# Performance work log

Measured on AMD Instinct MI355X. Metric: run time of the kernel, lower is better.

## Reference

```python
import jax, jax.numpy as jnp
import numpy as np

DF = 16
B, D, H, W = 2, 64, 64, 64


def _shift(a, axis, s):
    """Return a shifted so out[i] = a[i+s] along `axis`, zero-padded."""
    pad = [(0, 0)] * a.ndim
    pad[axis] = (1, 1)
    ap = jnp.pad(a, pad)
    idx = [slice(None)] * a.ndim
    idx[axis] = slice(1 + s, 1 + s + a.shape[axis])
    return ap[tuple(idx)]


def _image_grad(x, sum_axis):
    """Faithful replica of ImageGradient's (buggy) dense kernel.

    Uses only input channel 1; central difference along W; summed over the
    3 taps along `sum_axis` (1=D for pos==1, 2=H for pos==2); result is
    identical across all output channels.
    x: [B, C, D, H, W] -> [B, C, D, H, W]
    """
    s = x[:, 1]  # [B, D, H, W]
    g = 0.5 * (_shift(s, 3, 1) - _shift(s, 3, -1))  # d/dW central diff
    g3 = _shift(g, sum_axis, -1) + g + _shift(g, sum_axis, 1)
    return jnp.broadcast_to(g3[:, None], x.shape)


def _pconv(x, w, b):
    """nn.Conv3d(cin, cout, 1, padding=1): zero-pad spatial dims then 1x1x1 conv."""
    xp = jnp.pad(x, ((0, 0), (0, 0), (1, 1), (1, 1), (1, 1)))
    return jnp.einsum('bcdhw,oc->bodhw', xp, w) + b[None, :, None, None, None]


def setup_inputs() -> dict:
    key = jax.random.key(0)
    ks = jax.random.split(key, 8)
    p = jax.random.normal(ks[0], (B, DF, D, H, W), dtype=jnp.float32)
    q = jax.random.normal(ks[1], (B, DF, D, H, W), dtype=jnp.float32)
    W1 = jax.random.normal(ks[2], (DF, 6 * DF), dtype=jnp.float32) / np.sqrt(6 * DF)
    b1 = jax.random.normal(ks[3], (DF,), dtype=jnp.float32) * 0.01
    W2 = jax.random.normal(ks[4], (DF, DF), dtype=jnp.float32) / np.sqrt(DF)
    b2 = jax.random.normal(ks[5], (DF,), dtype=jnp.float32) * 0.01
    W3 = jax.random.normal(ks[6], (1, DF), dtype=jnp.float32) / np.sqrt(DF)
    b3 = jax.random.normal(ks[7], (1,), dtype=jnp.float32) * 0.01
    return {"p": p, "q": q, "W1": W1, "b1": b1, "W2": W2, "b2": b2, "W3": W3, "b3": b3}


def reference(p, q, W1, b1, W2, b2, W3, b3):
    dpx = _image_grad(p, 1)  # gradx: pos==1, sum over kd (D axis)
    dpy = _image_grad(p, 2)  # grady: pos==2, sum over kh (H axis)
    dqx = _image_grad(q, 1)
    dqy = _image_grad(q, 2)
    h = jnp.concatenate([p, dpx, dpy, q, dqx, dqy], axis=1)  # [B, 6*DF, D, H, W]
    h = jax.nn.relu(_pconv(h, W1, b1))  # [B, DF, D+2, H+2, W+2]
    h = jax.nn.relu(_pconv(h, W2, b2))  # [B, DF, D+4, H+4, W+4]
    h = jax.nn.relu(_pconv(h, W3, b3))  # [B, 1, D+6, H+6, W+6]
    return (h, p, dpx, dpy, q, dqx, dqy)
```

## Files before the change

### kernel.cpp

```cpp
#include <hip/hip_runtime.h>

#define N3   (64*64*64)
#define NO   70
#define NO2  (NO*NO)
#define NO3  (NO*NO*NO)
#define OH   (2*NO3)
#define SZ   (2*16*N3)

typedef __attribute__((ext_vector_type(4))) float f4;

__device__ __forceinline__ float relu(float x){ return x > 0.f ? x : 0.f; }

__global__ __launch_bounds__(256) void ham_interior(
    const float* __restrict__ p, const float* __restrict__ q,
    const float* __restrict__ W1, const float* __restrict__ b1,
    const float* __restrict__ W2, const float* __restrict__ b2,
    const float* __restrict__ W3, const float* __restrict__ b3p,
    float* __restrict__ out)
{
    __shared__ float WpT[16][16];
    __shared__ float WqT[16][16];
    __shared__ float W2l[16][16];
    __shared__ float b1l[16], b2l[16], W3l[16];
    __shared__ float s1x[16], s1y[16], s2x[16], s2y[16];

    int t = threadIdx.x;
    {
        int o = t >> 4, c = t & 15;
        WpT[c][o] = W1[o*96 + c];
        WqT[c][o] = W1[o*96 + 48 + c];
        W2l[o][c] = W2[o*16 + c];
    }
    if (t < 16) {
        b1l[t] = b1[t]; b2l[t] = b2[t]; W3l[t] = W3[t];
        float ax=0.f, ay=0.f, bx=0.f, by=0.f;
        #pragma unroll
        for (int j = 0; j < 16; ++j) {
            ax += W1[t*96 + 16 + j];
            ay += W1[t*96 + 32 + j];
            bx += W1[t*96 + 64 + j];
            by += W1[t*96 + 80 + j];
        }
        s1x[t]=ax; s1y[t]=ay; s2x[t]=bx; s2y[t]=by;
    }
    __syncthreads();

    int i  = blockIdx.x * 256 + t;
    int w4 = i & 15;  int w0 = w4 << 2;
    int r  = i >> 4;
    int h0 = r & 63;  r >>= 6;
    int d0 = r & 63;  int b = r >> 6;

    float b3v = b3p[0];

    const float* ps = p + (b*16 + 1)*N3;
    const float* qs = q + (b*16 + 1)*N3;

    auto row6 = [&](const float* s, int dd, int hh, float rr[6]) {
        if ((unsigned)dd >= 64u || (unsigned)hh >= 64u) {
            #pragma unroll
            for (int j = 0; j < 6; ++j) rr[j] = 0.f;
            return;
        }
        const float* rp = s + dd*4096 + hh*64 + w0;
        f4 v = *(const f4*)rp;
        rr[1]=v[0]; rr[2]=v[1]; rr[3]=v[2]; rr[4]=v[3];
        rr[0] = (w4 > 0)  ? rp[-1] : 0.f;
        rr[5] = (w4 < 15) ? rp[4]  : 0.f;
    };

    float dpx[4], dpy[4], dqx[4], dqy[4];
    {
        float rc[6], ra[6], rb[6], gc[4];
        row6(ps, d0,   h0,   rc);
        row6(ps, d0-1, h0,   ra);
        row6(ps, d0+1, h0,   rb);
        #pragma unroll
        for (int j = 0; j < 4; ++j) gc[j]  = 0.5f*(rc[j+2]-rc[j]);
        #pragma unroll
        for (int j = 0; j < 4; ++j) dpx[j] = 0.5f*(ra[j+2]-ra[j]) + gc[j] + 0.5f*(rb[j+2]-rb[j]);
        row6(ps, d0, h0-1, ra);
        row6(ps, d0, h0+1, rb);
        #pragma unroll
        for (int j = 0; j < 4; ++j) dpy[j] = 0.5f*(ra[j+2]-ra[j]) + gc[j] + 0.5f*(rb[j+2]-rb[j]);

        row6(qs, d0,   h0,   rc);
        row6(qs, d0-1, h0,   ra);
        row6(qs, d0+1, h0,   rb);
        #pragma unroll
        for (int j = 0; j < 4; ++j) gc[j]  = 0.5f*(rc[j+2]-rc[j]);
        #pragma unroll
        for (int j = 0; j < 4; ++j) dqx[j] = 0.5f*(ra[j+2]-ra[j]) + gc[j] + 0.5f*(rb[j+2]-rb[j]);
        row6(qs, d0, h0-1, ra);
        row6(qs, d0, h0+1, rb);
        #pragma unroll
        for (int j = 0; j < 4; ++j) dqy[j] = 0.5f*(ra[j+2]-ra[j]) + gc[j] + 0.5f*(rb[j+2]-rb[j]);
    }

    float y1[4][16];
    #pragma unroll
    for (int j = 0; j < 4; ++j)
        #pragma unroll
        for (int o = 0; o < 16; ++o)
            y1[j][o] = b1l[o] + s1x[o]*dpx[j] + s1y[o]*dpy[j]
                              + s2x[o]*dqx[j] + s2y[o]*dqy[j];

    int ibase = b*16*N3 + d0*4096 + h0*64 + w0;

    float* outp  = out + OH;
    float* outdx = out + OH + SZ;
    float* outdy = out + OH + 2*SZ;
    float* outq  = out + OH + 3*SZ;
    float* outqx = out + OH + 4*SZ;
    float* outqy = out + OH + 5*SZ;

    #pragma unroll
    for (int c = 0; c < 16; ++c) {
        f4 pc = *(const f4*)(p + ibase + c*N3);
        f4 qc = *(const f4*)(q + ibase + c*N3);
        __builtin_nontemporal_store(pc, (f4*)(outp + ibase + c*N3));
        __builtin_nontemporal_store(qc, (f4*)(outq + ibase + c*N3));
        #pragma unroll
        for (int o = 0; o < 16; ++o) {
            float wp = WpT[c][o], wq = WqT[c][o];
            #pragma unroll
            for (int j = 0; j < 4; ++j)
                y1[j][o] += wp*pc[j] + wq*qc[j];
        }
    }

    f4 vdx, vdy, vqx, vqy;
    #pragma unroll
    for (int j = 0; j < 4; ++j) { vdx[j]=dpx[j]; vdy[j]=dpy[j]; vqx[j]=dqx[j]; vqy[j]=dqy[j]; }
    #pragma unroll
    for (int c = 0; c < 16; ++c) {
        __builtin_nontemporal_store(vdx, (f4*)(outdx + ibase + c*N3));
        __builtin_nontemporal_store(vdy, (f4*)(outdy + ibase + c*N3));
        __builtin_nontemporal_store(vqx, (f4*)(outqx + ibase + c*N3));
        __builtin_nontemporal_store(vqy, (f4*)(outqy + ibase + c*N3));
    }

    int obase = b*NO3 + (d0+3)*NO2 + (h0+3)*NO + (w0+3);
    #pragma unroll
    for (int j = 0; j < 4; ++j) {
        float acc = b3v;
        #pragma unroll
        for (int o = 0; o < 16; ++o) {
            float a2 = b2l[o];
            #pragma unroll
            for (int c = 0; c < 16; ++c) a2 += W2l[o][c]*relu(y1[j][c]);
            acc += W3l[o]*relu(a2);
        }
        out[obase + j] = relu(acc);
    }
}

__global__ __launch_bounds__(256) void ham_border(
    const float* __restrict__ b1, const float* __restrict__ W2,
    const float* __restrict__ b2, const float* __restrict__ W3,
    const float* __restrict__ b3p, float* __restrict__ out)
{
    int i = blockIdx.x * 256 + threadIdx.x;
    if (i >= OH) return;

    int b = i / NO3;
    int r = i - b*NO3;
    int d = r / NO2; r -= d*NO2;
    int h = r / NO;
    int w = r - h*NO;
    (void)b;

    if ((unsigned)(d-3) < 64u && (unsigned)(h-3) < 64u && (unsigned)(w-3) < 64u) return;

    float b3v = b3p[0];
    float val;
    if ((unsigned)(d-1) >= 68u || (unsigned)(h-1) >= 68u || (unsigned)(w-1) >= 68u) {
        val = relu(b3v);
    } else if ((unsigned)(d-2) >= 66u || (unsigned)(h-2) >= 66u || (unsigned)(w-2) >= 66u) {
        float acc = b3v;
        #pragma unroll
        for (int o = 0; o < 16; ++o) acc += W3[o]*relu(b2[o]);
        val = relu(acc);
    } else {
        float acc = b3v;
        #pragma unroll
        for (int o = 0; o < 16; ++o) {
            float a2 = b2[o];
            #pragma unroll
            for (int c = 0; c < 16; ++c) a2 += W2[o*16 + c]*relu(b1[c]);
            acc += W3[o]*relu(a2);
        }
        val = relu(acc);
    }
    out[i] = val;
}

extern "C" void kernel_launch(void* const* d_in, const int* in_sizes, int n_in,
                              void* d_out, int out_size, void* d_ws, size_t ws_size,
                              hipStream_t stream) {
    const float* p  = (const float*)d_in[0];
    const float* q  = (const float*)d_in[1];
    const float* W1 = (const float*)d_in[2];
    const float* b1 = (const float*)d_in[3];
    const float* W2 = (const float*)d_in[4];
    const float* b2 = (const float*)d_in[5];
    const float* W3 = (const float*)d_in[6];
    const float* b3 = (const float*)d_in[7];
    float* out = (float*)d_out;

    ham_interior<<<512, 256, 0, stream>>>(p, q, W1, b1, W2, b2, W3, b3, out);
    ham_border<<<(OH + 255)/256, 256, 0, stream>>>(b1, W2, b2, W3, b3, out);
}
```

Baseline: 380.5 us.

## Fuse interior and border kernels into one launch and restructure store order

Merges the border-fill kernel into the interior kernel by giving the extra blocks a separate code path, so only one launch is issued. It also switches the nontemporal stores to plain stores, reorders work so the gradient outputs are written before the p/q copy loop to shorten register live ranges, and adds an occupancy hint of 4 blocks per CU to launch bounds. The aim is to remove the second launch's overhead and tail, and to get more waves in flight on the store-bound interior. Plain stores may pollute the cache, and the occupancy hint may cause register spills given the 64-float accumulator.

```diff
diff --git a/kernel.cpp b/kernel.cpp
--- a/kernel.cpp
+++ b/kernel.cpp
@@ -7,24 +7,61 @@
 #define OH   (2*NO3)
 #define SZ   (2*16*N3)
 
+#define INT_BLOCKS 512
+#define BRD_BLOCKS ((OH + 255) / 256)
+
 typedef __attribute__((ext_vector_type(4))) float f4;
 
 __device__ __forceinline__ float relu(float x){ return x > 0.f ? x : 0.f; }
 
-__global__ __launch_bounds__(256) void ham_interior(
+__global__ __launch_bounds__(256, 4) void ham_fused(
     const float* __restrict__ p, const float* __restrict__ q,
     const float* __restrict__ W1, const float* __restrict__ b1,
     const float* __restrict__ W2, const float* __restrict__ b2,
     const float* __restrict__ W3, const float* __restrict__ b3p,
     float* __restrict__ out)
 {
+    int t = threadIdx.x;
+
+    if (blockIdx.x >= INT_BLOCKS) {
+        int i = (blockIdx.x - INT_BLOCKS) * 256 + t;
+        if (i >= OH) return;
+        int r = i % NO3;
+        int d = r / NO2; r -= d*NO2;
+        int h = r / NO;
+        int w = r - h*NO;
+        if ((unsigned)(d-3) < 64u && (unsigned)(h-3) < 64u && (unsigned)(w-3) < 64u)
+            return;
+        float b3v = b3p[0];
+        float val;
+        if ((unsigned)(d-1) >= 68u || (unsigned)(h-1) >= 68u || (unsigned)(w-1) >= 68u) {
+            val = relu(b3v);
+        } else if ((unsigned)(d-2) >= 66u || (unsigned)(h-2) >= 66u || (unsigned)(w-2) >= 66u) {
+            float acc = b3v;
+            #pragma unroll
+            for (int o = 0; o < 16; ++o) acc += W3[o]*relu(b2[o]);
+            val = relu(acc);
+        } else {
+            float acc = b3v;
+            #pragma unroll
+            for (int o = 0; o < 16; ++o) {
+                float a2 = b2[o];
+                #pragma unroll
+                for (int c = 0; c < 16; ++c) a2 += W2[o*16 + c]*relu(b1[c]);
+                acc += W3[o]*relu(a2);
+            }
+            val = relu(acc);
+        }
+        out[i] = val;
+        return;
+    }
+
     __shared__ float WpT[16][16];
     __shared__ float WqT[16][16];
     __shared__ float W2l[16][16];
     __shared__ float b1l[16], b2l[16], W3l[16];
     __shared__ float s1x[16], s1y[16], s2x[16], s2y[16];
 
-    int t = threadIdx.x;
     {
         int o = t >> 4, c = t & 15;
         WpT[c][o] = W1[o*96 + c];
@@ -50,8 +87,6 @@
     int r  = i >> 4;
     int h0 = r & 63;  r >>= 6;
     int d0 = r & 63;  int b = r >> 6;
-
-    float b3v = b3p[0];
 
     const float* ps = p + (b*16 + 1)*N3;
     const float* qs = q + (b*16 + 1)*N3;
@@ -69,77 +104,78 @@
         rr[5] = (w4 < 15) ? rp[4]  : 0.f;
     };
 
-    float dpx[4], dpy[4], dqx[4], dqy[4];
+    float y1[4][16];
+    int ibase = b*16*N3 + d0*4096 + h0*64 + w0;
+
     {
-        float rc[6], ra[6], rb[6], gc[4];
-        row6(ps, d0,   h0,   rc);
-        row6(ps, d0-1, h0,   ra);
-        row6(ps, d0+1, h0,   rb);
-        #pragma unroll
-        for (int j = 0; j < 4; ++j) gc[j]  = 0.5f*(rc[j+2]-rc[j]);
-        #pragma unroll
-        for (int j = 0; j < 4; ++j) dpx[j] = 0.5f*(ra[j+2]-ra[j]) + gc[j] + 0.5f*(rb[j+2]-rb[j]);
-        row6(ps, d0, h0-1, ra);
-        row6(ps, d0, h0+1, rb);
-        #pragma unroll
-        for (int j = 0; j < 4; ++j) dpy[j] = 0.5f*(ra[j+2]-ra[j]) + gc[j] + 0.5f*(rb[j+2]-rb[j]);
-
-        row6(qs, d0,   h0,   rc);
-        row6(qs, d0-1, h0,   ra);
-        row6(qs, d0+1, h0,   rb);
-        #pragma unroll
-        for (int j = 0; j < 4; ++j) gc[j]  = 0.5f*(rc[j+2]-rc[j]);
-        #pragma unroll
-        for (int j = 0; j < 4; ++j) dqx[j] = 0.5f*(ra[j+2]-ra[j]) + gc[j] + 0.5f*(rb[j+2]-rb[j]);
-        row6(qs, d0, h0-1, ra);
-        row6(qs, d0, h0+1, rb);
-        #pragma unroll
-        for (int j = 0; j < 4; ++j) dqy[j] = 0.5f*(ra[j+2]-ra[j]) + gc[j] + 0.5f*(rb[j+2]-rb[j]);
-    }
-
-    float y1[4][16];
-    #pragma unroll
-    for (int j = 0; j < 4; ++j)
-        #pragma unroll
-        for (int o = 0; o < 16; ++o)
-            y1[j][o] = b1l[o] + s1x[o]*dpx[j] + s1y[o]*dpy[j]
-                              + s2x[o]*dqx[j] + s2y[o]*dqy[j];
-
-    int ibase = b*16*N3 + d0*4096 + h0*64 + w0;
-
-    float* outp  = out + OH;
-    float* outdx = out + OH + SZ;
-    float* outdy = out + OH + 2*SZ;
-    float* outq  = out + OH + 3*SZ;
-    float* outqx = out + OH + 4*SZ;
-    float* outqy = out + OH + 5*SZ;
-
-    #pragma unroll
-    for (int c = 0; c < 16; ++c) {
-        f4 pc = *(const f4*)(p + ibase + c*N3);
-        f4 qc = *(const f4*)(q + ibase + c*N3);
-        __builtin_nontemporal_store(pc, (f4*)(outp + ibase + c*N3));
-        __builtin_nontemporal_store(qc, (f4*)(outq + ibase + c*N3));
-        #pragma unroll
-        for (int o = 0; o < 16; ++o) {
-            float wp = WpT[c][o], wq = WqT[c][o];
-            #pragma unroll
-            for (int j = 0; j < 4; ++j)
-                y1[j][o] += wp*pc[j] + wq*qc[j];
-        }
-    }
-
-    f4 vdx, vdy, vqx, vqy;
-    #pragma unroll
-    for (int j = 0; j < 4; ++j) { vdx[j]=dpx[j]; vdy[j]=dpy[j]; vqx[j]=dqx[j]; vqy[j]=dqy[j]; }
-    #pragma unroll
-    for (int c = 0; c < 16; ++c) {
-        __builtin_nontemporal_store(vdx, (f4*)(outdx + ibase + c*N3));
-        __builtin_nontemporal_store(vdy, (f4*)(outdy + ibase + c*N3));
-        __builtin_nontemporal_store(vqx, (f4*)(outqx + ibase + c*N3));
-        __builtin_nontemporal_store(vqy, (f4*)(outqy + ibase + c*N3));
-    }
-
+        f4 vdx, vdy, vqx, vqy;
+        {
+            float rc[6], ra[6], rb[6], gc[4];
+            row6(ps, d0,   h0,   rc);
+            row6(ps, d0-1, h0,   ra);
+            row6(ps, d0+1, h0,   rb);
+            #pragma unroll
+            for (int j = 0; j < 4; ++j) gc[j]  = 0.5f*(rc[j+2]-rc[j]);
+            #pragma unroll
+            for (int j = 0; j < 4; ++j) vdx[j] = 0.5f*(ra[j+2]-ra[j]) + gc[j] + 0.5f*(rb[j+2]-rb[j]);
+            row6(ps, d0, h0-1, ra);
+            row6(ps, d0, h0+1, rb);
+            #pragma unroll
+            for (int j = 0; j < 4; ++j) vdy[j] = 0.5f*(ra[j+2]-ra[j]) + gc[j] + 0.5f*(rb[j+2]-rb[j]);
+
+            row6(qs, d0,   h0,   rc);
+            row6(qs, d0-1, h0,   ra);
+            row6(qs, d0+1, h0,   rb);
+            #pragma unroll
+            for (int j = 0; j < 4; ++j) gc[j]  = 0.5f*(rc[j+2]-rc[j]);
+            #pragma unroll
+            for (int j = 0; j < 4; ++j) vqx[j] = 0.5f*(ra[j+2]-ra[j]) + gc[j] + 0.5f*(rb[j+2]-rb[j]);
+            row6(qs, d0, h0-1, ra);
+            row6(qs, d0, h0+1, rb);
+            #pragma unroll
+            for (int j = 0; j < 4; ++j) vqy[j] = 0.5f*(ra[j+2]-ra[j]) + gc[j] + 0.5f*(rb[j+2]-rb[j]);
+        }
+
+        #pragma unroll
+        for (int j = 0; j < 4; ++j)
+            #pragma unroll
+            for (int o = 0; o < 16; ++o)
+                y1[j][o] = b1l[o] + s1x[o]*vdx[j] + s1y[o]*vdy[j]
+                                  + s2x[o]*vqx[j] + s2y[o]*vqy[j];
+
+        float* outdx = out + OH + SZ;
+        float* outdy = out + OH + 2*SZ;
+        float* outqx = out + OH + 4*SZ;
+        float* outqy = out + OH + 5*SZ;
+        #pragma unroll
+        for (int c = 0; c < 16; ++c) {
+            *(f4*)(outdx + ibase + c*N3) = vdx;
+            *(f4*)(outdy + ibase + c*N3) = vdy;
+            *(f4*)(outqx + ibase + c*N3) = vqx;
+            *(f4*)(outqy + ibase + c*N3) = vqy;
+        }
+    }
+
+    {
+        float* outp = out + OH;
+        float* outq = out + OH + 3*SZ;
+        #pragma unroll
+        for (int c = 0; c < 16; ++c) {
+            f4 pc = *(const f4*)(p + ibase + c*N3);
+            f4 qc = *(const f4*)(q + ibase + c*N3);
+            *(f4*)(outp + ibase + c*N3) = pc;
+            *(f4*)(outq + ibase + c*N3) = qc;
+            #pragma unroll
+            for (int o = 0; o < 16; ++o) {
+                float wp = WpT[c][o], wq = WqT[c][o];
+                #pragma unroll
+                for (int j = 0; j < 4; ++j)
+                    y1[j][o] += wp*pc[j] + wq*qc[j];
+            }
+        }
+    }
+
+    float b3v = b3p[0];
     int obase = b*NO3 + (d0+3)*NO2 + (h0+3)*NO + (w0+3);
     #pragma unroll
     for (int j = 0; j < 4; ++j) {
@@ -153,46 +189,6 @@
         }
         out[obase + j] = relu(acc);
     }
-}
-
-__global__ __launch_bounds__(256) void ham_border(
-    const float* __restrict__ b1, const float* __restrict__ W2,
-    const float* __restrict__ b2, const float* __restrict__ W3,
-    const float* __restrict__ b3p, float* __restrict__ out)
-{
-    int i = blockIdx.x * 256 + threadIdx.x;
-    if (i >= OH) return;
-
-    int b = i / NO3;
-    int r = i - b*NO3;
-    int d = r / NO2; r -= d*NO2;
-    int h = r / NO;
-    int w = r - h*NO;
-    (void)b;
-
-    if ((unsigned)(d-3) < 64u && (unsigned)(h-3) < 64u && (unsigned)(w-3) < 64u) return;
-
-    float b3v = b3p[0];
-    float val;
-    if ((unsigned)(d-1) >= 68u || (unsigned)(h-1) >= 68u || (unsigned)(w-1) >= 68u) {
-        val = relu(b3v);
-    } else if ((unsigned)(d-2) >= 66u || (unsigned)(h-2) >= 66u || (unsigned)(w-2) >= 66u) {
-        float acc = b3v;
-        #pragma unroll
-        for (int o = 0; o < 16; ++o) acc += W3[o]*relu(b2[o]);
-        val = relu(acc);
-    } else {
-        float acc = b3v;
-        #pragma unroll
-        for (int o = 0; o < 16; ++o) {
-            float a2 = b2[o];
-            #pragma unroll
-            for (int c = 0; c < 16; ++c) a2 += W2[o*16 + c]*relu(b1[c]);
-            acc += W3[o]*relu(a2);
-        }
-        val = relu(acc);
-    }
-    out[i] = val;
 }
 
 extern "C" void kernel_launch(void* const* d_in, const int* in_sizes, int n_in,
@@ -208,6 +204,6 @@
     const float* b3 = (const float*)d_in[7];
     float* out = (float*)d_out;
 
-    ham_interior<<<512, 256, 0, stream>>>(p, q, W1, b1, W2, b2, W3, b3, out);
-    ham_border<<<(OH + 255)/256, 256, 0, stream>>>(b1, W2, b2, W3, b3, out);
+    ham_fused<<<INT_BLOCKS + BRD_BLOCKS, 256, 0, stream>>>(
+        p, q, W1, b1, W2, b2, W3, b3, out);
 }
```

New measurement: 605.3 us. +59.1%, slower.
